# Performance work log

Measured on AMD Instinct MI355X. Metric: run time of the kernel, lower is better.

## Reference

```python
import jax, jax.numpy as jnp
import numpy as np

B, L, S = 8192, 1024, 3
OUTSIDE, TM_HELIX, INSIDE = 0, 1, 2


def setup_inputs() -> dict:
    key = jax.random.key(0)
    k1, k2 = jax.random.split(key)
    emissions = jax.random.normal(k1, (B, L, S), dtype=jnp.float32)
    tags = jax.random.randint(k2, (B, L), 0, S)
    mask = jnp.ones((B, L), dtype=jnp.float32)
    t = np.zeros((S, S), dtype=np.float32)
    t[OUTSIDE, INSIDE] = -5.0
    t[INSIDE, OUTSIDE] = -5.0
    t[OUTSIDE, TM_HELIX] = 1.0
    t[INSIDE, TM_HELIX] = 1.0
    t[TM_HELIX, OUTSIDE] = 1.0
    t[TM_HELIX, INSIDE] = 1.0
    transitions = jnp.asarray(t)
    return {"emissions": emissions, "mask": mask, "transitions": transitions, "tags": tags}


def _score_sentence(emissions, tags, mask, transitions):
    # emission score of the gold tag at every position: (B, L)
    em_score = jnp.take_along_axis(emissions, tags[..., None], axis=2)[..., 0]
    # transition score between consecutive gold tags: (B, L-1)
    trans_score = transitions[tags[:, :-1], tags[:, 1:]]
    return em_score[:, 0] * mask[:, 0] + jnp.sum(
        (trans_score + em_score[:, 1:]) * mask[:, 1:], axis=1
    )


def _forward_alg(emissions, mask, transitions):
    def step(alpha, xs):
        em_t, m_t = xs  # (B, S), (B,)
        # scores[b, i, j] = alpha[b, i] + T[i, j] + em_t[b, j]
        scores = alpha[:, :, None] + transitions[None, :, :] + em_t[:, None, :]
        new_alpha = jax.nn.logsumexp(scores, axis=1)
        alpha = jnp.where(m_t[:, None] > 0, new_alpha, alpha)
        return alpha, None

    alpha0 = emissions[:, 0, :]
    xs = (jnp.swapaxes(emissions[:, 1:, :], 0, 1),  # (L-1, B, S)
          jnp.swapaxes(mask[:, 1:], 0, 1))          # (L-1, B)
    alpha, _ = jax.lax.scan(step, alpha0, xs)
    return jax.nn.logsumexp(alpha, axis=1)  # (B,)


def reference(emissions, mask, transitions, tags):
    logZ = _forward_alg(emissions, mask, transitions)
    gold = _score_sentence(emissions, tags, mask, transitions)
    return jnp.mean(logZ - gold)
```

## Files before the change

### kernel.cpp

```cpp
#include <hip/hip_runtime.h>


#define LOG2E 1.4426950408889634f
#define LN2   0.6931471805599453f

constexpr int B = 8192;
constexpr int L = 1024;
constexpr int SEQS_PER_BLOCK = 4;

__device__ __forceinline__ float fexp2(float x) { return __builtin_amdgcn_exp2f(x); }
__device__ __forceinline__ float flog2(float x) { return __builtin_amdgcn_logf(x); }

__device__ __forceinline__ float f4get(const float4& v, int c) {
  return c == 0 ? v.x : (c == 1 ? v.y : (c == 2 ? v.z : v.w));
}
__device__ __forceinline__ int i4get(const int4& v, int c) {
  return c == 0 ? v.x : (c == 1 ? v.y : (c == 2 ? v.z : v.w));
}

__device__ __forceinline__ float mux3(float x0, float x1, float x2, int i) {
  return (i == 0) ? x0 : ((i == 1) ? x1 : x2);
}
__device__ __forceinline__ float trmux(const float* __restrict__ T2, int p, int c) {
  const float r0 = mux3(T2[0], T2[1], T2[2], c);
  const float r1 = mux3(T2[3], T2[4], T2[5], c);
  const float r2 = mux3(T2[6], T2[7], T2[8], c);
  return mux3(r0, r1, r2, p);
}

__device__ __forceinline__ void matmul3(float* __restrict__ D,
                                        const float* __restrict__ A,
                                        const float* __restrict__ Bm) {
  #pragma unroll
  for (int i = 0; i < 3; ++i)
    #pragma unroll
    for (int j = 0; j < 3; ++j)
      D[i * 3 + j] = A[i * 3 + 0] * Bm[0 * 3 + j] +
                     A[i * 3 + 1] * Bm[1 * 3 + j] +
                     A[i * 3 + 2] * Bm[2 * 3 + j];
}

__device__ __forceinline__ void renorm3(float* __restrict__ P, float& scale) {
  float m = P[0];
  #pragma unroll
  for (int e = 1; e < 9; ++e) m = fmaxf(m, P[e]);
  int ex;
  (void)frexpf(m, &ex);
  #pragma unroll
  for (int e = 0; e < 9; ++e) P[e] = ldexpf(P[e], -ex);
  scale += (float)ex;
}

__global__ __launch_bounds__(256, 4) void crf_main(
    const float* __restrict__ em, const float* __restrict__ mask,
    const float* __restrict__ trans, const int* __restrict__ tags,
    float* __restrict__ out) {
  const int lane = threadIdx.x & 63;
  const int wid = threadIdx.x >> 6;
  const int b = blockIdx.x * SEQS_PER_BLOCK + wid;

  const float4* em4 = (const float4*)(em + (size_t)b * (L * 3)) + lane * 12;
  const float4* mk4 = (const float4*)(mask + (size_t)b * L) + lane * 4;
  const int4*   tg4 = (const int4*)(tags + (size_t)b * L) + lane * 4;

  float4 E[12];
  #pragma unroll
  for (int u = 0; u < 12; ++u) E[u] = em4[u];
  float4 MK[4];
  #pragma unroll
  for (int u = 0; u < 4; ++u) MK[u] = mk4[u];
  int4 TG[4];
  #pragma unroll
  for (int u = 0; u < 4; ++u) TG[u] = tg4[u];

  float T2[9], tk[9];
  #pragma unroll
  for (int e = 0; e < 9; ++e) {
    T2[e] = trans[e] * LOG2E;
    tk[e] = fexp2(T2[e]);
  }

  float P[9] = {1.f, 0.f, 0.f, 0.f, 1.f, 0.f, 0.f, 0.f, 1.f};
  float scale = 0.f, gold = 0.f;
  float a0 = 0.f, a1 = 0.f, a2 = 0.f;
  float e0_sel = 0.f, mk0 = 0.f;
  int tag0 = 0, prev = 0;

  #pragma unroll
  for (int s = 0; s < 16; ++s) {
    const float ev0 = f4get(E[(3 * s + 0) >> 2], (3 * s + 0) & 3) * LOG2E;
    const float ev1 = f4get(E[(3 * s + 1) >> 2], (3 * s + 1) & 3) * LOG2E;
    const float ev2 = f4get(E[(3 * s + 2) >> 2], (3 * s + 2) & 3) * LOG2E;
    const float m   = f4get(MK[s >> 2], s & 3);
    const int   cur = i4get(TG[s >> 2], s & 3);

    const float e = mux3(ev0, ev1, ev2, cur);
    if (s == 0) {
      e0_sel = e; mk0 = m; tag0 = cur;
    } else {
      gold = fmaf(trmux(T2, prev, cur) + e, m, gold);
    }
    prev = cur;

    const float w0 = fexp2(ev0);
    const float w1 = fexp2(ev1);
    const float w2 = fexp2(ev2);
    if (s == 0) { a0 = w0; a1 = w1; a2 = w2; }
    const bool act = (m > 0.f) && !(s == 0 && lane == 0);
    const float g  = act ? 1.f : 0.f;
    const float c1 = 1.f - g;
    const float u0 = w0 * g, u1 = w1 * g, u2 = w2 * g;
    float M[9];
    M[0] = fmaf(tk[0], u0, c1); M[1] = tk[1] * u1;           M[2] = tk[2] * u2;
    M[3] = tk[3] * u0;          M[4] = fmaf(tk[4], u1, c1);  M[5] = tk[5] * u2;
    M[6] = tk[6] * u0;          M[7] = tk[7] * u1;           M[8] = fmaf(tk[8], u2, c1);
    float N[9];
    matmul3(N, P, M);
    #pragma unroll
    for (int e2 = 0; e2 < 9; ++e2) P[e2] = N[e2];

    if (s == 7 || s == 15) renorm3(P, scale);
  }

  const int prevLast = __shfl_up(prev, 1);
  if (lane == 0) gold = fmaf(e0_sel, mk0, gold);
  else           gold = fmaf(trmux(T2, prevLast, tag0) + e0_sel, mk0, gold);
  #pragma unroll
  for (int d = 1; d < 64; d <<= 1) gold += __shfl_xor(gold, d, 64);

  #pragma unroll
  for (int d = 1; d < 64; d <<= 1) {
    float o[9];
    #pragma unroll
    for (int e = 0; e < 9; ++e) o[e] = __shfl_xor(P[e], d, 64);
    const float osc = __shfl_xor(scale, d, 64);
    const bool later = (lane & d) != 0;
    float A[9], Bm[9];
    #pragma unroll
    for (int e = 0; e < 9; ++e) {
      A[e]  = later ? o[e] : P[e];
      Bm[e] = later ? P[e] : o[e];
    }
    float N[9];
    matmul3(N, A, Bm);
    #pragma unroll
    for (int e = 0; e < 9; ++e) P[e] = N[e];
    scale += osc;
  }

  __shared__ float red[SEQS_PER_BLOCK];
  if (lane == 0) {
    const float z = a0 * (P[0] + P[1] + P[2]) +
                    a1 * (P[3] + P[4] + P[5]) +
                    a2 * (P[6] + P[7] + P[8]);
    red[wid] = LN2 * (scale + flog2(z) - gold);
  }
  __syncthreads();
  if (threadIdx.x == 0) {
    const float s = red[0] + red[1] + red[2] + red[3];
    atomicAdd(out, s * (1.0f / (float)B));
  }
}

extern "C" void kernel_launch(void* const* d_in, const int* in_sizes, int n_in,
                              void* d_out, int out_size, void* d_ws, size_t ws_size,
                              hipStream_t stream) {
  const float* em    = (const float*)d_in[0];
  const float* mask  = (const float*)d_in[1];
  const float* trans = (const float*)d_in[2];
  const int*   tags  = (const int*)d_in[3];
  float* out = (float*)d_out;

  hipMemsetAsync(out, 0, sizeof(float), stream);
  crf_main<<<B / SEQS_PER_BLOCK, 256, 0, stream>>>(em, mask, trans, tags, out);
}
```

Measured before the change: 195.0 us.

## Stage per-sequence loads through LDS for coalesced global reads

Global loads for emissions, mask and tags are changed from per-lane strided float4 chunks to fully coalesced wave-contiguous loads. The data is transposed through padded shared memory in four rounds, and the next round's global loads are prefetched while the current round is written. Tags are packed into a 2-bit register word, and the transition lookup for the gold score becomes a shared-memory table index instead of a select chain. This adds LDS traffic, LDS capacity use and explicit waitcnt barriers, which may limit occupancy.

```diff
diff --git a/kernel.cpp b/kernel.cpp
--- a/kernel.cpp
+++ b/kernel.cpp
@@ -14,18 +14,9 @@
 __device__ __forceinline__ float f4get(const float4& v, int c) {
   return c == 0 ? v.x : (c == 1 ? v.y : (c == 2 ? v.z : v.w));
 }
-__device__ __forceinline__ int i4get(const int4& v, int c) {
-  return c == 0 ? v.x : (c == 1 ? v.y : (c == 2 ? v.z : v.w));
-}
 
 __device__ __forceinline__ float mux3(float x0, float x1, float x2, int i) {
   return (i == 0) ? x0 : ((i == 1) ? x1 : x2);
-}
-__device__ __forceinline__ float trmux(const float* __restrict__ T2, int p, int c) {
-  const float r0 = mux3(T2[0], T2[1], T2[2], c);
-  const float r1 = mux3(T2[3], T2[4], T2[5], c);
-  const float r2 = mux3(T2[6], T2[7], T2[8], c);
-  return mux3(r0, r1, r2, p);
 }
 
 __device__ __forceinline__ void matmul3(float* __restrict__ D,
@@ -59,46 +50,93 @@
   const int wid = threadIdx.x >> 6;
   const int b = blockIdx.x * SEQS_PER_BLOCK + wid;
 
-  const float4* em4 = (const float4*)(em + (size_t)b * (L * 3)) + lane * 12;
-  const float4* mk4 = (const float4*)(mask + (size_t)b * L) + lane * 4;
-  const int4*   tg4 = (const int4*)(tags + (size_t)b * L) + lane * 4;
+  __shared__ float4 sEm[SEQS_PER_BLOCK][16][13];
+  __shared__ float4 sMk[SEQS_PER_BLOCK][16][5];
+  __shared__ int4   sTg[SEQS_PER_BLOCK][16][5];
+  __shared__ float  sT2[12];
+  __shared__ float  red[SEQS_PER_BLOCK];
+
+  if (threadIdx.x < 9) sT2[threadIdx.x] = trans[threadIdx.x] * LOG2E;
+  __syncthreads();
+
+  const float4* emG = (const float4*)em + (size_t)b * 768;
+  const float4* mkG = (const float4*)mask + (size_t)b * 256;
+  const int4*   tgG = (const int4*)tags + (size_t)b * 256;
+
+  int wrow[3], wcol[3];
+  #pragma unroll
+  for (int c = 0; c < 3; ++c) {
+    const int m = 64 * c + lane;
+    wrow[c] = m / 12;
+    wcol[c] = m - 12 * wrow[c];
+  }
+  const int grp = lane >> 4;
+  const int cl = lane & 15;
+  const int mrow = lane >> 2, mcol = lane & 3;
 
   float4 E[12];
-  #pragma unroll
-  for (int u = 0; u < 12; ++u) E[u] = em4[u];
-  float4 MK[4];
-  #pragma unroll
-  for (int u = 0; u < 4; ++u) MK[u] = mk4[u];
-  int4 TG[4];
-  #pragma unroll
-  for (int u = 0; u < 4; ++u) TG[u] = tg4[u];
-
-  float T2[9], tk[9];
-  #pragma unroll
-  for (int e = 0; e < 9; ++e) {
-    T2[e] = trans[e] * LOG2E;
-    tk[e] = fexp2(T2[e]);
-  }
+  float4 MKv[4];
+  unsigned tpack = 0;
+
+  float4 e0 = emG[lane], e1 = emG[64 + lane], e2 = emG[128 + lane];
+  float4 mk = mkG[lane];
+  int4   tg = tgG[lane];
+  #pragma unroll
+  for (int p = 0; p < 4; ++p) {
+    float4 f0, f1, f2, fm;
+    int4 ft;
+    if (p < 3) {
+      f0 = emG[192 * (p + 1) + lane];
+      f1 = emG[192 * (p + 1) + 64 + lane];
+      f2 = emG[192 * (p + 1) + 128 + lane];
+      fm = mkG[64 * (p + 1) + lane];
+      ft = tgG[64 * (p + 1) + lane];
+    }
+    if (p) asm volatile("s_waitcnt lgkmcnt(0)" ::: "memory");
+    sEm[wid][wrow[0]][wcol[0]] = e0;
+    sEm[wid][wrow[1]][wcol[1]] = e1;
+    sEm[wid][wrow[2]][wcol[2]] = e2;
+    sMk[wid][mrow][mcol] = mk;
+    sTg[wid][mrow][mcol] = tg;
+    asm volatile("s_waitcnt lgkmcnt(0)" ::: "memory");
+    if (grp == p) {
+      #pragma unroll
+      for (int u = 0; u < 12; ++u) E[u] = sEm[wid][cl][u];
+      #pragma unroll
+      for (int u = 0; u < 4; ++u) MKv[u] = sMk[wid][cl][u];
+      #pragma unroll
+      for (int u = 0; u < 4; ++u) {
+        const int4 t = sTg[wid][cl][u];
+        tpack |= (unsigned)(t.x | (t.y << 2) | (t.z << 4) | (t.w << 6)) << (8 * u);
+      }
+    }
+    if (p < 3) { e0 = f0; e1 = f1; e2 = f2; mk = fm; tg = ft; }
+  }
+
+  float tk[9];
+  #pragma unroll
+  for (int e = 0; e < 9; ++e) tk[e] = fexp2(trans[e] * LOG2E);
 
   float P[9] = {1.f, 0.f, 0.f, 0.f, 1.f, 0.f, 0.f, 0.f, 1.f};
   float scale = 0.f, gold = 0.f;
   float a0 = 0.f, a1 = 0.f, a2 = 0.f;
   float e0_sel = 0.f, mk0 = 0.f;
-  int tag0 = 0, prev = 0;
+  const int tag0 = tpack & 3;
+  int prev = 0;
 
   #pragma unroll
   for (int s = 0; s < 16; ++s) {
     const float ev0 = f4get(E[(3 * s + 0) >> 2], (3 * s + 0) & 3) * LOG2E;
     const float ev1 = f4get(E[(3 * s + 1) >> 2], (3 * s + 1) & 3) * LOG2E;
     const float ev2 = f4get(E[(3 * s + 2) >> 2], (3 * s + 2) & 3) * LOG2E;
-    const float m   = f4get(MK[s >> 2], s & 3);
-    const int   cur = i4get(TG[s >> 2], s & 3);
+    const float m   = f4get(MKv[s >> 2], s & 3);
+    const int   cur = (tpack >> (2 * s)) & 3;
 
     const float e = mux3(ev0, ev1, ev2, cur);
     if (s == 0) {
-      e0_sel = e; mk0 = m; tag0 = cur;
+      e0_sel = e; mk0 = m;
     } else {
-      gold = fmaf(trmux(T2, prev, cur) + e, m, gold);
+      gold = fmaf(sT2[3 * prev + cur] + e, m, gold);
     }
     prev = cur;
 
@@ -123,8 +161,8 @@
   }
 
   const int prevLast = __shfl_up(prev, 1);
-  if (lane == 0) gold = fmaf(e0_sel, mk0, gold);
-  else           gold = fmaf(trmux(T2, prevLast, tag0) + e0_sel, mk0, gold);
+  const float t0 = sT2[3 * prevLast + tag0];
+  gold = fmaf((lane == 0 ? 0.f : t0) + e0_sel, mk0, gold);
   #pragma unroll
   for (int d = 1; d < 64; d <<= 1) gold += __shfl_xor(gold, d, 64);
 
@@ -148,7 +186,6 @@
     scale += osc;
   }
 
-  __shared__ float red[SEQS_PER_BLOCK];
   if (lane == 0) {
     const float z = a0 * (P[0] + P[1] + P[2]) +
                     a1 * (P[3] + P[4] + P[5]) +
```

Result: slower. 201.1 us (+3.1%).

## Stream inputs in chunks and cut register pressure to double occupancy

Applied to the files above, without the earlier changes.

Instead of preloading all 16 positions' emissions, masks and tags into registers, each lane now loads one group of four positions at a time inside a non-unrolled loop. Transition logits move to shared memory and are indexed directly rather than selected through mux chains. Launch bounds are raised to 8 blocks per CU, and the gold reduction is folded into the matrix scan loop, which is no longer unrolled. The aim is more waves in flight to hide memory latency on this bandwidth-bound kernel, at the cost of less load batching per wave and the risk of register spills under the tighter bound.

```diff
diff --git a/kernel.cpp b/kernel.cpp
--- a/kernel.cpp
+++ b/kernel.cpp
@@ -14,30 +14,9 @@
 __device__ __forceinline__ float f4get(const float4& v, int c) {
   return c == 0 ? v.x : (c == 1 ? v.y : (c == 2 ? v.z : v.w));
 }
-__device__ __forceinline__ int i4get(const int4& v, int c) {
-  return c == 0 ? v.x : (c == 1 ? v.y : (c == 2 ? v.z : v.w));
-}
 
 __device__ __forceinline__ float mux3(float x0, float x1, float x2, int i) {
   return (i == 0) ? x0 : ((i == 1) ? x1 : x2);
-}
-__device__ __forceinline__ float trmux(const float* __restrict__ T2, int p, int c) {
-  const float r0 = mux3(T2[0], T2[1], T2[2], c);
-  const float r1 = mux3(T2[3], T2[4], T2[5], c);
-  const float r2 = mux3(T2[6], T2[7], T2[8], c);
-  return mux3(r0, r1, r2, p);
-}
-
-__device__ __forceinline__ void matmul3(float* __restrict__ D,
-                                        const float* __restrict__ A,
-                                        const float* __restrict__ Bm) {
-  #pragma unroll
-  for (int i = 0; i < 3; ++i)
-    #pragma unroll
-    for (int j = 0; j < 3; ++j)
-      D[i * 3 + j] = A[i * 3 + 0] * Bm[0 * 3 + j] +
-                     A[i * 3 + 1] * Bm[1 * 3 + j] +
-                     A[i * 3 + 2] * Bm[2 * 3 + j];
 }
 
 __device__ __forceinline__ void renorm3(float* __restrict__ P, float& scale) {
@@ -51,7 +30,7 @@
   scale += (float)ex;
 }
 
-__global__ __launch_bounds__(256, 4) void crf_main(
+__global__ __launch_bounds__(256, 8) void crf_main(
     const float* __restrict__ em, const float* __restrict__ mask,
     const float* __restrict__ trans, const int* __restrict__ tags,
     float* __restrict__ out) {
@@ -59,26 +38,18 @@
   const int wid = threadIdx.x >> 6;
   const int b = blockIdx.x * SEQS_PER_BLOCK + wid;
 
-  const float4* em4 = (const float4*)(em + (size_t)b * (L * 3)) + lane * 12;
-  const float4* mk4 = (const float4*)(mask + (size_t)b * L) + lane * 4;
-  const int4*   tg4 = (const int4*)(tags + (size_t)b * L) + lane * 4;
+  __shared__ float sT2[12];
+  __shared__ float red[SEQS_PER_BLOCK];
+  if (threadIdx.x < 9) sT2[threadIdx.x] = trans[threadIdx.x] * LOG2E;
+  __syncthreads();
 
-  float4 E[12];
+  const float4* emp = (const float4*)(em + (size_t)b * (L * 3)) + lane * 12;
+  const float4* mkp = (const float4*)(mask + (size_t)b * L) + lane * 4;
+  const int4*   tgp = (const int4*)(tags + (size_t)b * L) + lane * 4;
+
+  float tk[9];
   #pragma unroll
-  for (int u = 0; u < 12; ++u) E[u] = em4[u];
-  float4 MK[4];
-  #pragma unroll
-  for (int u = 0; u < 4; ++u) MK[u] = mk4[u];
-  int4 TG[4];
-  #pragma unroll
-  for (int u = 0; u < 4; ++u) TG[u] = tg4[u];
-
-  float T2[9], tk[9];
-  #pragma unroll
-  for (int e = 0; e < 9; ++e) {
-    T2[e] = trans[e] * LOG2E;
-    tk[e] = fexp2(T2[e]);
-  }
+  for (int e = 0; e < 9; ++e) tk[e] = fexp2(trans[e] * LOG2E);
 
   float P[9] = {1.f, 0.f, 0.f, 0.f, 1.f, 0.f, 0.f, 0.f, 1.f};
   float scale = 0.f, gold = 0.f;
@@ -86,54 +57,69 @@
   float e0_sel = 0.f, mk0 = 0.f;
   int tag0 = 0, prev = 0;
 
-  #pragma unroll
-  for (int s = 0; s < 16; ++s) {
-    const float ev0 = f4get(E[(3 * s + 0) >> 2], (3 * s + 0) & 3) * LOG2E;
-    const float ev1 = f4get(E[(3 * s + 1) >> 2], (3 * s + 1) & 3) * LOG2E;
-    const float ev2 = f4get(E[(3 * s + 2) >> 2], (3 * s + 2) & 3) * LOG2E;
-    const float m   = f4get(MK[s >> 2], s & 3);
-    const int   cur = i4get(TG[s >> 2], s & 3);
+  #pragma unroll 1
+  for (int g = 0; g < 4; ++g) {
+    const float4 E0 = emp[3 * g + 0];
+    const float4 E1 = emp[3 * g + 1];
+    const float4 E2 = emp[3 * g + 2];
+    const float4 MKg = mkp[g];
+    const int4 tg = tgp[g];
+    const int tp = tg.x | (tg.y << 2) | (tg.z << 4) | (tg.w << 6);
+    const float ev[12] = {E0.x, E0.y, E0.z, E0.w, E1.x, E1.y,
+                          E1.z, E1.w, E2.x, E2.y, E2.z, E2.w};
 
-    const float e = mux3(ev0, ev1, ev2, cur);
-    if (s == 0) {
-      e0_sel = e; mk0 = m; tag0 = cur;
-    } else {
-      gold = fmaf(trmux(T2, prev, cur) + e, m, gold);
+    #pragma unroll
+    for (int q = 0; q < 4; ++q) {
+      const float ev0 = ev[3 * q + 0] * LOG2E;
+      const float ev1 = ev[3 * q + 1] * LOG2E;
+      const float ev2 = ev[3 * q + 2] * LOG2E;
+      const float m   = f4get(MKg, q);
+      const int   cur = (tp >> (2 * q)) & 3;
+
+      const float e = mux3(ev0, ev1, ev2, cur);
+      if (q == 0) {
+        if (g == 0) { e0_sel = e; mk0 = m; tag0 = cur; }
+        else        gold = fmaf(sT2[3 * prev + cur] + e, m, gold);
+      } else {
+        gold = fmaf(sT2[3 * prev + cur] + e, m, gold);
+      }
+      prev = cur;
+
+      const float w0 = fexp2(ev0);
+      const float w1 = fexp2(ev1);
+      const float w2 = fexp2(ev2);
+      if (q == 0 && g == 0) { a0 = w0; a1 = w1; a2 = w2; }
+      const bool first = (q == 0) && (g == 0);
+      const bool act = (m > 0.f) && !(first && lane == 0);
+      const float gg = act ? 1.f : 0.f;
+      const float c1 = 1.f - gg;
+      const float u0 = w0 * gg, u1 = w1 * gg, u2 = w2 * gg;
+      float M[9];
+      M[0] = fmaf(tk[0], u0, c1); M[1] = tk[1] * u1;           M[2] = tk[2] * u2;
+      M[3] = tk[3] * u0;          M[4] = fmaf(tk[4], u1, c1);  M[5] = tk[5] * u2;
+      M[6] = tk[6] * u0;          M[7] = tk[7] * u1;           M[8] = fmaf(tk[8], u2, c1);
+      #pragma unroll
+      for (int i = 0; i < 3; ++i) {
+        const float p0 = P[3 * i + 0], p1 = P[3 * i + 1], p2 = P[3 * i + 2];
+        P[3 * i + 0] = p0 * M[0] + p1 * M[3] + p2 * M[6];
+        P[3 * i + 1] = p0 * M[1] + p1 * M[4] + p2 * M[7];
+        P[3 * i + 2] = p0 * M[2] + p1 * M[5] + p2 * M[8];
+      }
     }
-    prev = cur;
-
-    const float w0 = fexp2(ev0);
-    const float w1 = fexp2(ev1);
-    const float w2 = fexp2(ev2);
-    if (s == 0) { a0 = w0; a1 = w1; a2 = w2; }
-    const bool act = (m > 0.f) && !(s == 0 && lane == 0);
-    const float g  = act ? 1.f : 0.f;
-    const float c1 = 1.f - g;
-    const float u0 = w0 * g, u1 = w1 * g, u2 = w2 * g;
-    float M[9];
-    M[0] = fmaf(tk[0], u0, c1); M[1] = tk[1] * u1;           M[2] = tk[2] * u2;
-    M[3] = tk[3] * u0;          M[4] = fmaf(tk[4], u1, c1);  M[5] = tk[5] * u2;
-    M[6] = tk[6] * u0;          M[7] = tk[7] * u1;           M[8] = fmaf(tk[8], u2, c1);
-    float N[9];
-    matmul3(N, P, M);
-    #pragma unroll
-    for (int e2 = 0; e2 < 9; ++e2) P[e2] = N[e2];
-
-    if (s == 7 || s == 15) renorm3(P, scale);
+    if (g & 1) renorm3(P, scale);
   }
 
   const int prevLast = __shfl_up(prev, 1);
-  if (lane == 0) gold = fmaf(e0_sel, mk0, gold);
-  else           gold = fmaf(trmux(T2, prevLast, tag0) + e0_sel, mk0, gold);
-  #pragma unroll
-  for (int d = 1; d < 64; d <<= 1) gold += __shfl_xor(gold, d, 64);
+  const float t0 = sT2[3 * prevLast + tag0];
+  gold = fmaf((lane == 0 ? 0.f : t0) + e0_sel, mk0, gold);
 
-  #pragma unroll
+  #pragma unroll 1
   for (int d = 1; d < 64; d <<= 1) {
     float o[9];
     #pragma unroll
     for (int e = 0; e < 9; ++e) o[e] = __shfl_xor(P[e], d, 64);
     const float osc = __shfl_xor(scale, d, 64);
+    gold += __shfl_xor(gold, d, 64);
     const bool later = (lane & d) != 0;
     float A[9], Bm[9];
     #pragma unroll
@@ -141,14 +127,16 @@
       A[e]  = later ? o[e] : P[e];
       Bm[e] = later ? P[e] : o[e];
     }
-    float N[9];
-    matmul3(N, A, Bm);
     #pragma unroll
-    for (int e = 0; e < 9; ++e) P[e] = N[e];
+    for (int i = 0; i < 3; ++i) {
+      const float p0 = A[3 * i + 0], p1 = A[3 * i + 1], p2 = A[3 * i + 2];
+      P[3 * i + 0] = p0 * Bm[0] + p1 * Bm[3] + p2 * Bm[6];
+      P[3 * i + 1] = p0 * Bm[1] + p1 * Bm[4] + p2 * Bm[7];
+      P[3 * i + 2] = p0 * Bm[2] + p1 * Bm[5] + p2 * Bm[8];
+    }
     scale += osc;
   }
 
-  __shared__ float red[SEQS_PER_BLOCK];
   if (lane == 0) {
     const float z = a0 * (P[0] + P[1] + P[2]) +
                     a1 * (P[3] + P[4] + P[5]) +
```

Result: slower. 265.5 us (+36.1%).
